# Optimization experiments

Measured on AMD Instinct MI355X. Metric: run time of the kernel, lower is better.

Reference implementation:

```python
import jax, jax.numpy as jnp
import numpy as np


def _conv(x, w, b, pad_h=0):
    # x: [B,C,H,W_feat], w: [O,C,kh,1]; kernel width is 1 so this is a 1D conv along H
    y = jax.lax.conv_general_dilated(
        x, w, window_strides=(1, 1), padding=[(pad_h, pad_h), (0, 0)],
        dimension_numbers=('NCHW', 'OIHW', 'NCHW'))
    return y + b[None, :, None, None]


def _lin(x, w, b):
    # Semi_Linear: shared nn.Linear applied to the last axis of every [channel, height] slice.
    # Since the nested loops cover the full leading dims, this is one batched matmul.
    return jnp.einsum('bchi,oi->bcho', x, w) + b


def setup_inputs() -> dict:
    key = jax.random.key(0)
    ks = jax.random.split(key, 40)
    B = 4096
    rn = lambda k, shape, s=0.1: jax.random.normal(k, shape, jnp.float32) * s
    d = {}
    d['x'] = jax.random.normal(ks[0], (B, 1, 5, 127), jnp.float32)
    # block A params (first set of definitions in __init__)
    d['ca1_w'] = rn(ks[1], (5, 1, 3, 1));    d['ca1_b'] = rn(ks[2], (5,))
    d['l01_w'] = rn(ks[3], (81, 127));        d['l01_b'] = rn(ks[4], (81,))
    d['cb1_w'] = rn(ks[5], (25, 5, 3, 1));    d['cb1_b'] = rn(ks[6], (25,))
    d['cc1_w'] = rn(ks[7], (25, 1, 1, 1));    d['cc1_b'] = rn(ks[8], (25,))
    d['r01_w'] = rn(ks[9], (81, 127));        d['r01_b'] = rn(ks[10], (81,))
    # block B params
    d['c1_w'] = rn(ks[11], (75, 25, 2, 1));   d['c1_b'] = rn(ks[12], (75,))
    d['l1_w'] = rn(ks[13], (30, 81));         d['l1_b'] = rn(ks[14], (30,))
    d['c2_w'] = rn(ks[15], (125, 75, 2, 1));  d['c2_b'] = rn(ks[16], (125,))
    d['ca_w'] = rn(ks[17], (125, 25, 3, 1));  d['ca_b'] = rn(ks[18], (125,))
    d['ra_w'] = rn(ks[19], (30, 81));         d['ra_b'] = rn(ks[20], (30,))
    # block C params (second, overriding set of definitions)
    d['ca2_w'] = rn(ks[21], (25, 125, 2, 1)); d['ca2_b'] = rn(ks[22], (25,))
    d['l02_w'] = rn(ks[23], (10, 30));        d['l02_b'] = rn(ks[24], (10,))
    d['cb2_w'] = rn(ks[25], (1, 25, 2, 1));   d['cb2_b'] = rn(ks[26], (1,))
    d['cc2_w'] = rn(ks[27], (1, 125, 1, 1));  d['cc2_b'] = rn(ks[28], (1,))
    d['r02_w'] = rn(ks[29], (10, 30));        d['r02_b'] = rn(ks[30], (10,))
    d['fl_w'] = rn(ks[31], (1, 10));          d['fl_b'] = rn(ks[32], (1,))
    return d


def reference(x, ca1_w, ca1_b, l01_w, l01_b, cb1_w, cb1_b, cc1_w, cc1_b, r01_w, r01_b,
              c1_w, c1_b, l1_w, l1_b, c2_w, c2_b, ca_w, ca_b, ra_w, ra_b,
              ca2_w, ca2_b, l02_w, l02_b, cb2_w, cb2_b, cc2_w, cc2_b, r02_w, r02_b,
              fl_w, fl_b):
    # block A
    z = _conv(x, ca1_w, ca1_b, pad_h=1)            # [B,5,5,127]
    z = jax.nn.relu(_lin(z, l01_w, l01_b))         # [B,5,5,81]
    z = _conv(z, cb1_w, cb1_b, pad_h=1)            # [B,25,5,81]
    y = _lin(x, r01_w, r01_b)                      # [B,1,5,81]
    y = _conv(y, cc1_w, cc1_b)                     # [B,25,5,81]
    x1 = z + y
    # block B
    z = _conv(x1, c1_w, c1_b)                      # [B,75,4,81]
    z = jax.nn.relu(_lin(z, l1_w, l1_b))           # [B,75,4,30]
    z = _conv(z, c2_w, c2_b)                       # [B,125,3,30]
    y = _lin(x1, ra_w, ra_b)                       # [B,25,5,30]
    y = _conv(y, ca_w, ca_b)                       # [B,125,3,30]
    x2 = z + y
    # block C
    z = _conv(x2, ca2_w, ca2_b)                    # [B,25,2,30]
    z = jax.nn.relu(_lin(z, l02_w, l02_b))         # [B,25,2,10]
    z = _conv(z, cb2_w, cb2_b)                     # [B,1,1,10]
    y = _lin(x2, r02_w, r02_b)                     # [B,125,3,10]
    y = _conv(y, cc2_w, cc2_b)                     # [B,1,3,10]
    x3 = z + y                                     # broadcast -> [B,1,3,10]
    return _lin(x3, fl_w, fl_b)                    # [B,1,3,1]
```

## Files before the change

kernel.cpp:

```cpp
#include <hip/hip_runtime.h>


typedef unsigned short u16;
typedef __attribute__((ext_vector_type(8))) short bf16x8;
typedef __attribute__((ext_vector_type(4))) float f32x4;
typedef __attribute__((ext_vector_type(8))) unsigned short u16x8;
typedef __attribute__((ext_vector_type(2))) unsigned int u32x2;

__device__ __forceinline__ float bf2f(u16 u) {
  return __uint_as_float(((unsigned)u) << 16);
}
__device__ __forceinline__ u16 f2bf(float f) {
  unsigned u = __float_as_uint(f);
  return (u16)((u + 0x7FFFu + ((u >> 16) & 1u)) >> 16);
}

#define Z4 make_float4(0.f, 0.f, 0.f, 0.f)

#define OF_CS01   0
#define OF_CS1    81
#define OF_CSR    111
#define OF_CSAC   141
#define OF_CS02   266
#define OF_CSCC2  276
#define OF_L01T   280
#define OF_R01T   10948
#define OF_SWT    21616
#define OF_CB1T   26800
#define OF_C1T    27175
#define OF_SCT    30928
#define OF_CA2T   31528
#define OF_WT2    41528
#define OF_ZPAD   57912
#define F32_TOTAL 57920

#define R_XT   0
#define R_XL   635
#define R_YA   1040
#define R_ZA   1445
#define R_P    3470
#define R_Q    4970
#define R_V4A  5270
#define R_V1   11270
#define R_VRP  12770
#define R_TP   16520
#define R_X2   0
#define R_XJ   12770
#define ROWS_TOTAL 25520

struct Ctx {
  const float *x, *ca1_w, *ca1_b, *l01_b, *r01_b, *cb1_b, *cc1_w, *cc1_b;
  const float *c1_b, *l1_b, *c2_b, *ca_b, *ra_b, *ca2_b, *l02_b;
  const float *cb2_w, *cb2_b, *cc2_w, *cc2_b, *r02_b, *fl_w, *fl_b;
  const float *l01_w, *r01_w, *l1_w, *ra_w, *c1_w, *c2_w, *ca_w, *cb1_w;
  const float *l02_w, *r02_w, *ca2_w;
  float *F;
  float *zAcc;
  float *yAcc;
  u16 *A;
  float *out;
  int CB;
  int b0g;
};

__global__ __launch_bounds__(256) void k0c(Ctx C) {
  const int t0 = blockIdx.x * 256 + threadIdx.x;
  const int NT = 32 * 256;
  float* F = C.F;
  for (int k = t0; k < 277; k += NT) {
    float s = 0.f;
    if (k < 81)       { for (int i = 0; i < 127; ++i) s += C.l01_w[k * 127 + i]; F[OF_CS01 + k] = s; }
    else if (k < 111) { int j = k - 81;  for (int a = 0; a < 81; ++a) s += C.l1_w[j * 81 + a]; F[OF_CS1 + j] = s; }
    else if (k < 141) { int j = k - 111; for (int a = 0; a < 81; ++a) s += C.ra_w[j * 81 + a]; F[OF_CSR + j] = s; }
    else if (k < 266) { int o = k - 141; for (int i = 0; i < 75; ++i) s += C.ca_w[o * 75 + i]; F[OF_CSAC + o] = s; }
    else if (k < 276) { int q = k - 266; for (int j = 0; j < 30; ++j) s += C.l02_w[q * 30 + j]; F[OF_CS02 + q] = s; }
    else              { float ss = 0.f; for (int o = 0; o < 125; ++o) ss += C.cc2_w[o]; F[OF_CSCC2] = ss; }
  }
  for (int e = t0; e < 8; e += NT) F[OF_ZPAD + e] = 0.f;
  for (int e = t0; e < 10668; e += NT) { int i = e / 84, a = e % 84;
    F[OF_L01T + e] = (a < 81) ? C.l01_w[a * 127 + i] : 0.f; }
  for (int e = t0; e < 10668; e += NT) { int i = e / 84, a = e % 84;
    F[OF_R01T + e] = (a < 81) ? C.r01_w[a * 127 + i] : 0.f; }
  for (int e = t0; e < 5184; e += NT)  { int a = e / 64, j2 = e % 64;
    F[OF_SWT + e] = (j2 < 30) ? C.l1_w[j2 * 81 + a]
                  : (j2 < 60) ? C.ra_w[(j2 - 30) * 81 + a] : 0.f; }
  for (int e = t0; e < 375; e += NT)   { int k = e / 25, c = e % 25; F[OF_CB1T + e] = C.cb1_w[c * 15 + k]; }
  for (int e = t0; e < 3750; e += NT)  { int k = e / 75, m = e % 75; F[OF_C1T + e] = C.c1_w[m * 50 + k]; }
  for (int e = t0; e < 600; e += NT)   { int j = e / 20, q2 = e % 20;
    F[OF_SCT + e] = (q2 < 10) ? C.l02_w[q2 * 30 + j] : C.r02_w[(q2 - 10) * 30 + j]; }
  for (int e = t0; e < 10000; e += NT) { int k = e / 40, r = e % 40, cg = r / 8, i = r % 8;
    F[OF_CA2T + e] = (i < 5) ? C.ca2_w[(cg * 5 + i) * 250 + k] : 0.f; }
  u16* WT2 = (u16*)(F + OF_WT2);
  for (int e = t0; e < 32768; e += NT) {
    int o = e >> 8, k = e & 255;
    float v = 0.f;
    if (o < 125) {
      if (k < 150) v = C.c2_w[o * 150 + k];
      else if (k >= 160 && k < 235) v = C.ca_w[o * 75 + (k - 160)];
    }
    WT2[e] = f2bf(v);
  }
}

__global__ __launch_bounds__(256) void k0t(Ctx C) {
  __shared__ float tile[64][65];
  const int tid = threadIdx.x;
  const int b0 = blockIdx.x * 64;
  const int i0 = blockIdx.y * 64;
  for (int e = tid; e < 64 * 64; e += 256) {
    int s = e >> 6, ii = e & 63, gi = i0 + ii;
    if (gi < 635) tile[s][ii] = C.x[(size_t)(C.b0g + b0 + s) * 635 + gi];
  }
  __syncthreads();
  const int lane = tid & 63, wv = tid >> 6;
  u16* xT = C.A + (size_t)R_XT * C.CB;
#pragma unroll
  for (int k = 0; k < 16; ++k) {
    int r = wv * 16 + k, gi = i0 + r;
    if (gi < 635) xT[(size_t)gi * C.CB + b0 + lane] = f2bf(tile[lane][r]);
  }
}

__global__ __launch_bounds__(256) void k1(Ctx C) {
  const int col = blockIdx.x * 256 + threadIdx.x;
  if (col >= C.CB) return;
  const int g = blockIdx.y, type = g / 15, r = g % 15, h = r / 3, a0 = (r % 3) * 28;
  const size_t cb = (size_t)C.CB;
  const u16* __restrict__ xT = C.A + (size_t)R_XT * cb;
  const float* __restrict__ wT = C.F + (type ? OF_R01T : OF_L01T) + a0;
  float4 A0=Z4,A1=Z4,A2=Z4,A3=Z4,A4=Z4,A5=Z4,A6=Z4;
  for (int i = 0; i < 127; ++i) {
    float xv = bf2f(xT[(size_t)(h * 127 + i) * cb + col]);
    const float4* __restrict__ W = (const float4*)(wT + i * 84);
#define K1F(Aq, P) { float4 w = W[P]; Aq.x += w.x*xv; Aq.y += w.y*xv; Aq.z += w.z*xv; Aq.w += w.w*xv; }
    K1F(A0,0) K1F(A1,1) K1F(A2,2) K1F(A3,3) K1F(A4,4) K1F(A5,5) K1F(A6,6)
#undef K1F
  }
  u16* dst = C.A + (size_t)(type ? R_YA : R_XL) * cb;
  auto wr = [&](int a, float v) {
    if (a < 81) {
      float rr = v + (type ? C.r01_b[a] : 0.f);
      dst[(size_t)(h * 81 + a) * cb + col] = f2bf(rr);
    }
  };
#define K1O(Aq, P) { wr(a0+4*P+0, Aq.x); wr(a0+4*P+1, Aq.y); wr(a0+4*P+2, Aq.z); wr(a0+4*P+3, Aq.w); }
  K1O(A0,0) K1O(A1,1) K1O(A2,2) K1O(A3,3) K1O(A4,4) K1O(A5,5) K1O(A6,6)
#undef K1O
}

__global__ __launch_bounds__(256) void k2(Ctx C) {
  const int col = blockIdx.x * 256 + threadIdx.x;
  if (col >= C.CB) return;
  const int g = blockIdx.y, c5 = g / 15, r = g % 15, h = r / 3, a0 = (r % 3) * 27;
  const u16* __restrict__ XL = C.A + (size_t)R_XL * C.CB;
  const float* __restrict__ F = C.F;
  float acc[27];
  float cb = C.ca1_b[c5];
#pragma unroll
  for (int a = 0; a < 27; ++a) acc[a] = cb * F[OF_CS01 + a0 + a] + C.l01_b[a0 + a];
#pragma unroll
  for (int dh = 0; dh < 3; ++dh) {
    int hp = h - 1 + dh;
    if (hp < 0 || hp > 4) continue;
    float w = C.ca1_w[c5 * 3 + dh];
#pragma unroll
    for (int a = 0; a < 27; ++a) acc[a] += w * bf2f(XL[(size_t)(hp * 81 + a0 + a) * C.CB + col]);
  }
  u16* zA = C.A + (size_t)R_ZA * C.CB;
#pragma unroll
  for (int a = 0; a < 27; ++a)
    zA[(size_t)((c5 * 5 + h) * 81 + a0 + a) * C.CB + col] = f2bf(fmaxf(acc[a], 0.f));
}

__global__ __launch_bounds__(256) void k3(Ctx C) {
  const int col = blockIdx.x * 256 + threadIdx.x;
  if (col >= C.CB) return;
  const int g = blockIdx.y, pair = g >> 1, j0 = (g & 1) * 32;
  const bool isP = (pair < 25);
  const size_t cb = (size_t)C.CB;
  const u16* __restrict__ src = C.A + (size_t)(isP ? (R_ZA + pair * 81) : (R_YA + (pair - 25) * 81)) * cb;
  const float* __restrict__ SWT = C.F + OF_SWT + j0;
  float4 A0=Z4,A1=Z4,A2=Z4,A3=Z4,A4=Z4,A5=Z4,A6=Z4,A7=Z4;
  for (int a = 0; a < 81; ++a) {
    float xv = bf2f(src[(size_t)a * cb + col]);
    const float4* __restrict__ W = (const float4*)(SWT + a * 64);
#define K3F(Aq, P) { float4 w = W[P]; Aq.x += w.x*xv; Aq.y += w.y*xv; Aq.z += w.z*xv; Aq.w += w.w*xv; }
    K3F(A0,0) K3F(A1,1) K3F(A2,2) K3F(A3,3) K3F(A4,4) K3F(A5,5) K3F(A6,6) K3F(A7,7)
#undef K3F
  }
  u16* dst = C.A + (size_t)(isP ? (R_P + pair * 60) : (R_Q + (pair - 25) * 60)) * cb;
  auto wr = [&](int j2, float v) {
    if (j2 < 60) dst[(size_t)j2 * cb + col] = f2bf(v);
  };
#define K3O(Aq, P) { wr(j0+4*P+0, Aq.x); wr(j0+4*P+1, Aq.y); wr(j0+4*P+2, Aq.z); wr(j0+4*P+3, Aq.w); }
  K3O(A0,0) K3O(A1,1) K3O(A2,2) K3O(A3,3) K3O(A4,4) K3O(A5,5) K3O(A6,6) K3O(A7,7)
#undef K3O
}

__global__ __launch_bounds__(256) void k4(Ctx C) {
  const int col = blockIdx.x * 256 + threadIdx.x;
  if (col >= C.CB) return;
  const int g = blockIdx.y, cg = g / 60, j2 = g % 60;
  const size_t cb = (size_t)C.CB;
  const u16* __restrict__ Pb = C.A + (size_t)R_P * cb;
  const u16* __restrict__ Qb = C.A + (size_t)R_Q * cb;
  const float* __restrict__ F = C.F;
  float sj = (j2 < 30) ? F[OF_CS1 + j2] : F[OF_CSR + (j2 - 30)];
  float acc[5][5];
#pragma unroll
  for (int cl = 0; cl < 5; ++cl) {
    int c = cg * 5 + cl;
    float base = (C.cb1_b[c] + C.cc1_b[c]) * sj;
    float cw = C.cc1_w[c];
#pragma unroll
    for (int h = 0; h < 5; ++h)
      acc[cl][h] = base + cw * bf2f(Qb[(size_t)(h * 60 + j2) * cb + col]);
  }
#pragma unroll
  for (int c5 = 0; c5 < 5; ++c5)
#pragma unroll
    for (int hp = 0; hp < 5; ++hp) {
      float pv = bf2f(Pb[(size_t)((c5 * 5 + hp) * 60 + j2) * cb + col]);
#pragma unroll
      for (int dh = 0; dh < 3; ++dh) {
        int h = hp + 1 - dh;
        if (h < 0 || h > 4) continue;
        const float* __restrict__ w = F + OF_CB1T + (c5 * 3 + dh) * 25 + cg * 5;
#pragma unroll
        for (int cl = 0; cl < 5; ++cl) acc[cl][h] += w[cl] * pv;
      }
    }
  u16* v4 = C.A + (size_t)R_V4A * cb;
  u16* v1 = C.A + (size_t)R_V1 * cb;
#pragma unroll
  for (int cl = 0; cl < 5; ++cl) {
    int row = (cg * 5 + cl) * 60 + j2;
    ushort4 pk;
    pk.x = f2bf(acc[cl][0]); pk.y = f2bf(acc[cl][1]);
    pk.z = f2bf(acc[cl][2]); pk.w = f2bf(acc[cl][3]);
    *(ushort4*)(v4 + ((size_t)row * cb + col) * 4) = pk;
    v1[(size_t)row * cb + col] = f2bf(acc[cl][4]);
  }
  if (j2 >= 30) {
    u16* vrp = C.A + (size_t)R_VRP * cb;
    int jr = j2 - 30;
#pragma unroll
    for (int cl = 0; cl < 5; ++cl) {
      int base = (cg * 5 + cl) * 30 + jr;
      vrp[(size_t)(base)        * cb + col] = f2bf(acc[cl][0]);
      vrp[(size_t)(base + 750)  * cb + col] = f2bf(acc[cl][1]);
      vrp[(size_t)(base + 1500) * cb + col] = f2bf(acc[cl][2]);
      vrp[(size_t)(base + 2250) * cb + col] = f2bf(acc[cl][3]);
      vrp[(size_t)(base + 3000) * cb + col] = f2bf(acc[cl][4]);
    }
  }
}

__global__ __launch_bounds__(256, 2) void k5(Ctx C) {
  const int col = blockIdx.x * 256 + threadIdx.x;
  if (col >= C.CB) return;
  const int g = blockIdx.y, mg = g / 30, j = g % 30;
  const size_t cb = (size_t)C.CB;
  const u16* __restrict__ v4 = C.A + (size_t)R_V4A * cb;
  const u16* __restrict__ v1 = C.A + (size_t)R_V1 * cb;
  const float* __restrict__ F = C.F;
  float s1 = F[OF_CS1 + j], lb = C.l1_b[j];
  float4 B0,B1,B2,B3,B4,B5,B6,B7,B8,B9,B10,B11,B12,B13,B14;
#define K5I(Bq, P) { float bb = C.c1_b[mg*15+P] * s1 + lb; Bq = make_float4(bb,bb,bb,bb); }
  K5I(B0,0) K5I(B1,1) K5I(B2,2) K5I(B3,3) K5I(B4,4) K5I(B5,5) K5I(B6,6) K5I(B7,7)
  K5I(B8,8) K5I(B9,9) K5I(B10,10) K5I(B11,11) K5I(B12,12) K5I(B13,13) K5I(B14,14)
#undef K5I
  for (int c = 0; c < 25; ++c) {
    int row = c * 60 + j;
    ushort4 pk = *(const ushort4*)(v4 + ((size_t)row * cb + col) * 4);
    float x0 = bf2f(pk.x), x1 = bf2f(pk.y), x2 = bf2f(pk.z), x3 = bf2f(pk.w);
    float x4 = bf2f(v1[(size_t)row * cb + col]);
    const float* __restrict__ wp0 = F + OF_C1T + (c * 2) * 75 + mg * 15;
    const float* __restrict__ wp1 = wp0 + 75;
#define K5F(Bq, P) { float w0v = wp0[P], w1v = wp1[P]; \
    Bq.x += w0v*x0 + w1v*x1; Bq.y += w0v*x1 + w1v*x2; \
    Bq.z += w0v*x2 + w1v*x3; Bq.w += w0v*x3 + w1v*x4; }
    K5F(B0,0) K5F(B1,1) K5F(B2,2) K5F(B3,3) K5F(B4,4) K5F(B5,5) K5F(B6,6) K5F(B7,7)
    K5F(B8,8) K5F(B9,9) K5F(B10,10) K5F(B11,11) K5F(B12,12) K5F(B13,13) K5F(B14,14)
#undef K5F
  }
  u16* tp = C.A + (size_t)R_TP * cb;
#define K5O(Bq, P) { int rb = (mg*15+P)*30 + j; \
    tp[(size_t)(rb)        * cb + col] = f2bf(fmaxf(Bq.x, 0.f)); \
    tp[(size_t)(rb + 2250) * cb + col] = f2bf(fmaxf(Bq.y, 0.f)); \
    tp[(size_t)(rb + 4500) * cb + col] = f2bf(fmaxf(Bq.z, 0.f)); \
    tp[(size_t)(rb + 6750) * cb + col] = f2bf(fmaxf(Bq.w, 0.f)); }
  K5O(B0,0) K5O(B1,1) K5O(B2,2) K5O(B3,3) K5O(B4,4) K5O(B5,5) K5O(B6,6) K5O(B7,7)
  K5O(B8,8) K5O(B9,9) K5O(B10,10) K5O(B11,11) K5O(B12,12) K5O(B13,13) K5O(B14,14)
#undef K5O
}

union CvtAF { u32x2 p[2]; bf16x8 v; };

#define RD(D, TA, OFF) asm volatile("ds_read_b64_tr_b16 %0, %1 offset:" OFF : "=&v"(D) : "v"(TA));
#define TRS_EVEN(TA) \
  RD(p00,TA,"0")     RD(p01,TA,"1024")  RD(p10,TA,"8192")  RD(p11,TA,"9216") \
  RD(p20,TA,"16384") RD(p21,TA,"17408") RD(p30,TA,"24576") RD(p31,TA,"25600") \
  RD(p40,TA,"32768") RD(p41,TA,"33792") RD(p50,TA,"40960") RD(p51,TA,"41984") \
  RD(p60,TA,"49152") RD(p61,TA,"50176") RD(p70,TA,"57344") RD(p71,TA,"58368")
#define TRS_ODD(TA) \
  RD(p00,TA,"128")   RD(p01,TA,"1152")  RD(p10,TA,"8320")  RD(p11,TA,"9344") \
  RD(p20,TA,"16512") RD(p21,TA,"17536") RD(p30,TA,"24704") RD(p31,TA,"25728") \
  RD(p40,TA,"32896") RD(p41,TA,"33920") RD(p50,TA,"41088") RD(p51,TA,"42112") \
  RD(p60,TA,"49280") RD(p61,TA,"50304") RD(p70,TA,"57472") RD(p71,TA,"58496")

__global__ __launch_bounds__(256, 2) void k6m(Ctx C) {
  __shared__ u16 sA[32768];
  const int tid = threadIdx.x;
  const int col0 = blockIdx.x * 128;
  const int gy = blockIdx.y;
  const int j = gy / 3, h3 = gy % 3;
  const size_t cb = (size_t)C.CB;
  const u16* __restrict__ A_ = C.A;
  const u16* __restrict__ WT2 = (const u16*)(C.F + OF_WT2);
  const float* __restrict__ F = C.F;

  const int x = tid & 63, wv = tid >> 6;
  const int klane = (x >> 1) & 3;
  const int m0s = ((x >> 3) << 4) + ((x & 1) << 3);
  const u16* zsrc = (const u16*)(F + OF_ZPAD);
#pragma unroll
  for (int p = 0; p < 16; ++p) {
    int k = p * 16 + wv * 4 + klane;
    const u16* src;
    bool pad = (k >= 150 && k < 160) || (k >= 235);
    if (pad) {
      src = zsrc;
    } else {
      int srow;
      if (k < 150) srow = R_TP + (h3 + (k & 1)) * 2250 + (k >> 1) * 30 + j;
      else { int kk = k - 160; int c = kk / 3; srow = R_VRP + (h3 + (kk - c * 3)) * 750 + c * 30 + j; }
      src = A_ + (size_t)srow * cb + col0 + m0s;
    }
    __builtin_amdgcn_global_load_lds(
        (const __attribute__((address_space(1))) void*)src,
        (__attribute__((address_space(3))) void*)&sA[(p * 4 + wv) * 512],
        16, 0, 0);
  }

  const int l = tid & 63, w = tid >> 6;
  const int lc = l & 15, q = l >> 4;
  const u16* wbA = WT2 + (size_t)(w * 32 + lc) * 256 + q * 8;
  const u16* wbB = WT2 + (size_t)(w * 32 + 16 + lc) * 256 + q * 8;
  bf16x8 b00 = *(const bf16x8*)(wbA + 0*32), b01 = *(const bf16x8*)(wbA + 1*32),
         b02 = *(const bf16x8*)(wbA + 2*32), b03 = *(const bf16x8*)(wbA + 3*32),
         b04 = *(const bf16x8*)(wbA + 4*32), b05 = *(const bf16x8*)(wbA + 5*32),
         b06 = *(const bf16x8*)(wbA + 6*32), b07 = *(const bf16x8*)(wbA + 7*32);
  bf16x8 b10 = *(const bf16x8*)(wbB + 0*32), b11 = *(const bf16x8*)(wbB + 1*32),
         b12 = *(const bf16x8*)(wbB + 2*32), b13 = *(const bf16x8*)(wbB + 3*32),
         b14 = *(const bf16x8*)(wbB + 4*32), b15 = *(const bf16x8*)(wbB + 5*32),
         b16 = *(const bf16x8*)(wbB + 6*32), b17 = *(const bf16x8*)(wbB + 7*32);

  float rbj = C.ra_b[j];
  u16* x2b = C.A + (size_t)R_X2 * cb;
  const size_t rowbase = (size_t)(h3 * 30 + j) * 125;
  const int o0 = w * 32 + lc;
  const int o1 = o0 + 16;
  const int o1c = (o1 < 125) ? o1 : 0;
  float bs0 = C.c2_b[o0] + C.ca_b[o0] + rbj * F[OF_CSAC + o0];
  float bs1 = C.c2_b[o1c] + C.ca_b[o1c] + rbj * F[OF_CSAC + o1c];

  __syncthreads();

  unsigned ldsbase = (unsigned)(size_t)(&sA[0]);
  const unsigned ta0 = ldsbase + (unsigned)((2 * q) * 1024 + lc * 8);
  const unsigned ta1 = ta0 + 256;
  const unsigned ta2 = ta0 + 512;
  const unsigned ta3 = ta0 + 768;

  u32x2 p00,p01, p10,p11, p20,p21, p30,p31, p40,p41, p50,p51, p60,p61, p70,p71;

  TRS_EVEN(ta0)

#define MM(FS, BA, BB) \
    a0 = __builtin_amdgcn_mfma_f32_16x16x32_bf16(FS, BA, a0, 0, 0, 0); \
    a1 = __builtin_amdgcn_mfma_f32_16x16x32_bf16(FS, BB, a1, 0, 0, 0);

#define MG_BODY(MG, ...) { \
    asm volatile("s_waitcnt lgkmcnt(0)" ::: "memory"); \
    __builtin_amdgcn_sched_barrier(0); \
    bf16x8 f0,f1,f2,f3,f4,f5,f6,f7; \
    { CvtAF c_; c_.p[0]=p00; c_.p[1]=p01; f0=c_.v; } \
    { CvtAF c_; c_.p[0]=p10; c_.p[1]=p11; f1=c_.v; } \
    { CvtAF c_; c_.p[0]=p20; c_.p[1]=p21; f2=c_.v; } \
    { CvtAF c_; c_.p[0]=p30; c_.p[1]=p31; f3=c_.v; } \
    { CvtAF c_; c_.p[0]=p40; c_.p[1]=p41; f4=c_.v; } \
    { CvtAF c_; c_.p[0]=p50; c_.p[1]=p51; f5=c_.v; } \
    { CvtAF c_; c_.p[0]=p60; c_.p[1]=p61; f6=c_.v; } \
    { CvtAF c_; c_.p[0]=p70; c_.p[1]=p71; f7=c_.v; } \
    __VA_ARGS__ \
    f32x4 a0 = {0.f,0.f,0.f,0.f}, a1 = {0.f,0.f,0.f,0.f}; \
    MM(f0,b00,b10) MM(f1,b01,b11) MM(f2,b02,b12) MM(f3,b03,b13) \
    MM(f4,b04,b14) MM(f5,b05,b15) MM(f6,b06,b16) MM(f7,b07,b17) \
    const int cw = col0 + (MG) * 16 + q * 4; \
    { ushort4 pk; pk.x = f2bf(a0[0]+bs0); pk.y = f2bf(a0[1]+bs0); \
      pk.z = f2bf(a0[2]+bs0); pk.w = f2bf(a0[3]+bs0); \
      *(ushort4*)(x2b + (rowbase + o0) * cb + cw) = pk; } \
    if (o1 < 125) { ushort4 pk; pk.x = f2bf(a1[0]+bs1); pk.y = f2bf(a1[1]+bs1); \
      pk.z = f2bf(a1[2]+bs1); pk.w = f2bf(a1[3]+bs1); \
      *(ushort4*)(x2b + (rowbase + o1) * cb + cw) = pk; } \
  }

  MG_BODY(0, TRS_ODD(ta0))
  MG_BODY(1, TRS_EVEN(ta1))
  MG_BODY(2, TRS_ODD(ta1))
  MG_BODY(3, TRS_EVEN(ta2))
  MG_BODY(4, TRS_ODD(ta2))
  MG_BODY(5, TRS_EVEN(ta3))
  MG_BODY(6, TRS_ODD(ta3))
  MG_BODY(7)
#undef MG_BODY
#undef MM
}

__global__ __launch_bounds__(256) void k7(Ctx C) {
  const int col = blockIdx.x * 256 + threadIdx.x;
  if (col >= C.CB) return;
  const int g = blockIdx.y;
  const int o = g / 3, h3 = g % 3;
  const size_t cb = (size_t)C.CB;
  const u16* __restrict__ x2b = C.A + (size_t)R_X2 * cb;
  const float* __restrict__ SCT = C.F + OF_SCT;
  float4 A0=Z4,A1=Z4,A2=Z4,A3=Z4,A4=Z4;
  for (int j = 0; j < 30; ++j) {
    float xv = bf2f(x2b[(size_t)((h3 * 30 + j) * 125 + o) * cb + col]);
    const float4* __restrict__ W = (const float4*)(SCT + j * 20);
#define K7F(Aq, P) { float4 w = W[P]; Aq.x += w.x*xv; Aq.y += w.y*xv; Aq.z += w.z*xv; Aq.w += w.w*xv; }
    K7F(A0,0) K7F(A1,1) K7F(A2,2) K7F(A3,3) K7F(A4,4)
#undef K7F
  }
  u16* XJ = C.A + (size_t)R_XJ * cb;
  auto wq = [&](int qq, float v) { XJ[(size_t)(g * 10 + qq) * cb + col] = f2bf(v); };
  wq(0,A0.x); wq(1,A0.y); wq(2,A0.z); wq(3,A0.w);
  wq(4,A1.x); wq(5,A1.y); wq(6,A1.z); wq(7,A1.w);
  wq(8,A2.x); wq(9,A2.y);
  float s = C.fl_w[0]*A2.z + C.fl_w[1]*A2.w
          + C.fl_w[2]*A3.x + C.fl_w[3]*A3.y + C.fl_w[4]*A3.z + C.fl_w[5]*A3.w
          + C.fl_w[6]*A4.x + C.fl_w[7]*A4.y + C.fl_w[8]*A4.z + C.fl_w[9]*A4.w;
  atomicAdd(&C.yAcc[(size_t)h3 * C.CB + col], C.cc2_w[o] * s);
}

__global__ __launch_bounds__(256) void k8a(Ctx C) {
  const int col = blockIdx.x * 256 + threadIdx.x;
  if (col >= C.CB) return;
  const int g = blockIdx.y, cg = g / 20, rem = g % 20, hh = rem / 10, q = rem % 10;
  const size_t cb = (size_t)C.CB;
  const u16* __restrict__ XJ = C.A + (size_t)R_XJ * cb;
  const float* __restrict__ F = C.F;
  float4 A0 = Z4; float a4 = 0.f;
  const float* __restrict__ Wb = F + OF_CA2T + cg * 8;
  for (int k = 0; k < 250; ++k) {
    int o = k >> 1, dh = k & 1;
    float xv = bf2f(XJ[(size_t)((o * 3 + hh + dh) * 10 + q) * cb + col]);
    const float* __restrict__ wr = Wb + k * 40;
    float4 w0 = *(const float4*)wr;
    float w4 = wr[4];
    A0.x += w0.x * xv; A0.y += w0.y * xv; A0.z += w0.z * xv; A0.w += w0.w * xv;
    a4 += w4 * xv;
  }
  float s02 = F[OF_CS02 + q];
  float lb = C.l02_b[q];
  const int c0 = cg * 5;
  float part = 0.f;
  {
    float zc;
    zc = fmaxf(A0.x + C.ca2_b[c0+0] * s02 + lb, 0.f); part += C.cb2_w[(c0+0)*2+hh] * zc;
    zc = fmaxf(A0.y + C.ca2_b[c0+1] * s02 + lb, 0.f); part += C.cb2_w[(c0+1)*2+hh] * zc;
    zc = fmaxf(A0.z + C.ca2_b[c0+2] * s02 + lb, 0.f); part += C.cb2_w[(c0+2)*2+hh] * zc;
    zc = fmaxf(A0.w + C.ca2_b[c0+3] * s02 + lb, 0.f); part += C.cb2_w[(c0+3)*2+hh] * zc;
    zc = fmaxf(a4   + C.ca2_b[c0+4] * s02 + lb, 0.f); part += C.cb2_w[(c0+4)*2+hh] * zc;
  }
  atomicAdd(&C.zAcc[col], C.fl_w[q] * part);
}

__global__ __launch_bounds__(256) void k8c(Ctx C) {
  const int col = blockIdx.x * 256 + threadIdx.x;
  if (col >= C.CB) return;
  float scc2 = C.F[OF_CSCC2];
  float cst = C.fl_b[0];
#pragma unroll
  for (int q = 0; q < 10; ++q)
    cst += C.fl_w[q] * (C.cb2_b[0] + C.r02_b[q] * scc2 + C.cc2_b[0]);
  float za = C.zAcc[col];
#pragma unroll
  for (int h = 0; h < 3; ++h)
    C.out[(size_t)(C.b0g + col) * 3 + h] = cst + za + C.yAcc[(size_t)h * C.CB + col];
}

extern "C" void kernel_launch(void* const* d_in, const int* in_sizes, int n_in,
                              void* d_out, int out_size, void* d_ws, size_t ws_size,
                              hipStream_t stream) {
  (void)n_in; (void)out_size;
  Ctx C;
  C.x     = (const float*)d_in[0];
  C.ca1_w = (const float*)d_in[1];  C.ca1_b = (const float*)d_in[2];
  C.l01_w = (const float*)d_in[3];  C.l01_b = (const float*)d_in[4];
  C.cb1_w = (const float*)d_in[5];  C.cb1_b = (const float*)d_in[6];
  C.cc1_w = (const float*)d_in[7];  C.cc1_b = (const float*)d_in[8];
  C.r01_w = (const float*)d_in[9];  C.r01_b = (const float*)d_in[10];
  C.c1_w  = (const float*)d_in[11]; C.c1_b  = (const float*)d_in[12];
  C.l1_w  = (const float*)d_in[13]; C.l1_b  = (const float*)d_in[14];
  C.c2_w  = (const float*)d_in[15]; C.c2_b  = (const float*)d_in[16];
  C.ca_w  = (const float*)d_in[17]; C.ca_b  = (const float*)d_in[18];
  C.ra_w  = (const float*)d_in[19]; C.ra_b  = (const float*)d_in[20];
  C.ca2_w = (const float*)d_in[21]; C.ca2_b = (const float*)d_in[22];
  C.l02_w = (const float*)d_in[23]; C.l02_b = (const float*)d_in[24];
  C.cb2_w = (const float*)d_in[25]; C.cb2_b = (const float*)d_in[26];
  C.cc2_w = (const float*)d_in[27]; C.cc2_b = (const float*)d_in[28];
  C.r02_w = (const float*)d_in[29]; C.r02_b = (const float*)d_in[30];
  C.fl_w  = (const float*)d_in[31]; C.fl_b  = (const float*)d_in[32];
  C.out   = (float*)d_out;

  const int B = in_sizes[0] / 635;

  int CB = 4096;
  if (CB > B) CB = B;
  size_t accoff, actoff;
  for (;;) {
    accoff = ((size_t)F32_TOTAL * 4 + 255) & ~(size_t)255;
    actoff = (accoff + (size_t)4 * CB * 4 + 255) & ~(size_t)255;
    if (CB <= 256 || actoff + (size_t)ROWS_TOTAL * CB * 2 <= ws_size) break;
    CB >>= 1;
  }
  C.F = (float*)d_ws;
  C.zAcc = (float*)((char*)d_ws + accoff);
  C.yAcc = C.zAcc + CB;
  C.A = (u16*)((char*)d_ws + actoff);
  C.CB = CB;

  C.b0g = 0;
  k0c<<<dim3(32), dim3(256), 0, stream>>>(C);

  const int bt64 = CB / 64, bt128 = CB / 128, bt256 = (CB + 255) / 256;
  for (int b0 = 0; b0 < B; b0 += CB) {
    C.b0g = b0;
    hipMemsetAsync(C.zAcc, 0, (size_t)4 * CB * sizeof(float), stream);
    k0t<<<dim3(bt64, 10),   dim3(256), 0, stream>>>(C);
    k1 <<<dim3(bt256, 30),  dim3(256), 0, stream>>>(C);
    k2 <<<dim3(bt256, 75),  dim3(256), 0, stream>>>(C);
    k3 <<<dim3(bt256, 60),  dim3(256), 0, stream>>>(C);
    k4 <<<dim3(bt256, 300), dim3(256), 0, stream>>>(C);
    k5 <<<dim3(bt256, 150), dim3(256), 0, stream>>>(C);
    k6m<<<dim3(bt128, 90),  dim3(256), 0, stream>>>(C);
    k7 <<<dim3(bt256, 375), dim3(256), 0, stream>>>(C);
    k8a<<<dim3(bt256, 100), dim3(256), 0, stream>>>(C);
    k8c<<<dim3(bt256, 1),   dim3(256), 0, stream>>>(C);
  }
}
```

Baseline: 324.8 us.

## Port block-B first conv (k5) to bf16 MFMA with LDS transposed reads

Replaces the scalar FMA implementation of the c1 conv (25->75 channels, kernel 2) with an MFMA-based kernel. Each block handles one (j, output-height) pair and 128 batch columns, and stages its 64-row K slab into LDS with global_load_lds. The slab is read back through ds_read_b64_tr_b16 and multiplied against prepacked bf16 c1 weights. The upstream k4 output layout changes to a single h-major VLP buffer, so the K rows for each output height are contiguous. This adds weight prepacking and K padding from 50 to 64, and wastes some MFMA work on padded output channels 75..79.

```diff
diff --git a/kernel.cpp b/kernel.cpp
--- a/kernel.cpp
+++ b/kernel.cpp
@@ -32,7 +32,8 @@
 #define OF_CA2T   31528
 #define OF_WT2    41528
 #define OF_ZPAD   57912
-#define F32_TOTAL 57920
+#define OF_C1W2   57920
+#define F32_TOTAL 60480
 
 #define R_XT   0
 #define R_XL   635
@@ -40,8 +41,7 @@
 #define R_ZA   1445
 #define R_P    3470
 #define R_Q    4970
-#define R_V4A  5270
-#define R_V1   11270
+#define R_VLP  5270
 #define R_VRP  12770
 #define R_TP   16520
 #define R_X2   0
@@ -85,7 +85,6 @@
     F[OF_SWT + e] = (j2 < 30) ? C.l1_w[j2 * 81 + a]
                   : (j2 < 60) ? C.ra_w[(j2 - 30) * 81 + a] : 0.f; }
   for (int e = t0; e < 375; e += NT)   { int k = e / 25, c = e % 25; F[OF_CB1T + e] = C.cb1_w[c * 15 + k]; }
-  for (int e = t0; e < 3750; e += NT)  { int k = e / 75, m = e % 75; F[OF_C1T + e] = C.c1_w[m * 50 + k]; }
   for (int e = t0; e < 600; e += NT)   { int j = e / 20, q2 = e % 20;
     F[OF_SCT + e] = (q2 < 10) ? C.l02_w[q2 * 30 + j] : C.r02_w[(q2 - 10) * 30 + j]; }
   for (int e = t0; e < 10000; e += NT) { int k = e / 40, r = e % 40, cg = r / 8, i = r % 8;
@@ -99,6 +98,12 @@
       else if (k >= 160 && k < 235) v = C.ca_w[o * 75 + (k - 160)];
     }
     WT2[e] = f2bf(v);
+  }
+  u16* C1W2 = (u16*)(F + OF_C1W2);
+  for (int e = t0; e < 5120; e += NT) {
+    int o = e >> 6, k = e & 63;
+    float v = (o < 75 && k < 50) ? C.c1_w[o * 50 + k] : 0.f;
+    C1W2[e] = f2bf(v);
   }
 }
 
@@ -230,72 +235,124 @@
         for (int cl = 0; cl < 5; ++cl) acc[cl][h] += w[cl] * pv;
       }
     }
-  u16* v4 = C.A + (size_t)R_V4A * cb;
-  u16* v1 = C.A + (size_t)R_V1 * cb;
-#pragma unroll
-  for (int cl = 0; cl < 5; ++cl) {
-    int row = (cg * 5 + cl) * 60 + j2;
-    ushort4 pk;
-    pk.x = f2bf(acc[cl][0]); pk.y = f2bf(acc[cl][1]);
-    pk.z = f2bf(acc[cl][2]); pk.w = f2bf(acc[cl][3]);
-    *(ushort4*)(v4 + ((size_t)row * cb + col) * 4) = pk;
-    v1[(size_t)row * cb + col] = f2bf(acc[cl][4]);
-  }
-  if (j2 >= 30) {
+  if (j2 < 30) {
+    u16* vlp = C.A + (size_t)R_VLP * cb;
+#pragma unroll
+    for (int cl = 0; cl < 5; ++cl) {
+      int base = (cg * 5 + cl) * 30 + j2;
+#pragma unroll
+      for (int h = 0; h < 5; ++h)
+        vlp[(size_t)(base + h * 750) * cb + col] = f2bf(acc[cl][h]);
+    }
+  } else {
     u16* vrp = C.A + (size_t)R_VRP * cb;
     int jr = j2 - 30;
 #pragma unroll
     for (int cl = 0; cl < 5; ++cl) {
       int base = (cg * 5 + cl) * 30 + jr;
-      vrp[(size_t)(base)        * cb + col] = f2bf(acc[cl][0]);
-      vrp[(size_t)(base + 750)  * cb + col] = f2bf(acc[cl][1]);
-      vrp[(size_t)(base + 1500) * cb + col] = f2bf(acc[cl][2]);
-      vrp[(size_t)(base + 2250) * cb + col] = f2bf(acc[cl][3]);
-      vrp[(size_t)(base + 3000) * cb + col] = f2bf(acc[cl][4]);
+#pragma unroll
+      for (int h = 0; h < 5; ++h)
+        vrp[(size_t)(base + h * 750) * cb + col] = f2bf(acc[cl][h]);
     }
   }
 }
 
-__global__ __launch_bounds__(256, 2) void k5(Ctx C) {
-  const int col = blockIdx.x * 256 + threadIdx.x;
-  if (col >= C.CB) return;
-  const int g = blockIdx.y, mg = g / 30, j = g % 30;
+union CvtAF { u32x2 p[2]; bf16x8 v; };
+
+__global__ __launch_bounds__(256, 2) void k5m(Ctx C) {
+  __shared__ u16 sA[8192];
+  const int tid = threadIdx.x;
+  const int col0 = blockIdx.x * 128;
+  const int gy = blockIdx.y;
+  const int j = gy >> 2, h4 = gy & 3;
   const size_t cb = (size_t)C.CB;
-  const u16* __restrict__ v4 = C.A + (size_t)R_V4A * cb;
-  const u16* __restrict__ v1 = C.A + (size_t)R_V1 * cb;
+  const u16* __restrict__ A_ = C.A;
+  const u16* __restrict__ WB = (const u16*)(C.F + OF_C1W2);
   const float* __restrict__ F = C.F;
+
+  const int x = tid & 63, wv = tid >> 6;
+  const int klane = (x >> 1) & 3;
+  const int m0s = ((x >> 3) << 4) + ((x & 1) << 3);
+  const u16* zsrc = (const u16*)(F + OF_ZPAD);
+#pragma unroll
+  for (int p = 0; p < 4; ++p) {
+    int k = p * 16 + wv * 4 + klane;
+    const u16* src;
+    if (k >= 50) {
+      src = zsrc;
+    } else {
+      int c = k >> 1, dc = k & 1;
+      int srow = R_VLP + (h4 + dc) * 750 + c * 30 + j;
+      src = A_ + (size_t)srow * cb + col0 + m0s;
+    }
+    __builtin_amdgcn_global_load_lds(
+        (const __attribute__((address_space(1))) void*)src,
+        (__attribute__((address_space(3))) void*)&sA[(p * 4 + wv) * 512],
+        16, 0, 0);
+  }
+
+  const int l = tid & 63, w = tid >> 6;
+  const int lc = l & 15, q = l >> 4;
+#define BF(N, S) (*(const bf16x8*)(WB + (size_t)((N)*16 + lc) * 64 + (S)*32 + q*8))
+  bf16x8 B00 = BF(0,0), B10 = BF(1,0), B20 = BF(2,0), B30 = BF(3,0), B40 = BF(4,0);
+  bf16x8 B01 = BF(0,1), B11 = BF(1,1), B21 = BF(2,1), B31 = BF(3,1), B41 = BF(4,1);
+#undef BF
   float s1 = F[OF_CS1 + j], lb = C.l1_b[j];
-  float4 B0,B1,B2,B3,B4,B5,B6,B7,B8,B9,B10,B11,B12,B13,B14;
-#define K5I(Bq, P) { float bb = C.c1_b[mg*15+P] * s1 + lb; Bq = make_float4(bb,bb,bb,bb); }
-  K5I(B0,0) K5I(B1,1) K5I(B2,2) K5I(B3,3) K5I(B4,4) K5I(B5,5) K5I(B6,6) K5I(B7,7)
-  K5I(B8,8) K5I(B9,9) K5I(B10,10) K5I(B11,11) K5I(B12,12) K5I(B13,13) K5I(B14,14)
-#undef K5I
-  for (int c = 0; c < 25; ++c) {
-    int row = c * 60 + j;
-    ushort4 pk = *(const ushort4*)(v4 + ((size_t)row * cb + col) * 4);
-    float x0 = bf2f(pk.x), x1 = bf2f(pk.y), x2 = bf2f(pk.z), x3 = bf2f(pk.w);
-    float x4 = bf2f(v1[(size_t)row * cb + col]);
-    const float* __restrict__ wp0 = F + OF_C1T + (c * 2) * 75 + mg * 15;
-    const float* __restrict__ wp1 = wp0 + 75;
-#define K5F(Bq, P) { float w0v = wp0[P], w1v = wp1[P]; \
-    Bq.x += w0v*x0 + w1v*x1; Bq.y += w0v*x1 + w1v*x2; \
-    Bq.z += w0v*x2 + w1v*x3; Bq.w += w0v*x3 + w1v*x4; }
-    K5F(B0,0) K5F(B1,1) K5F(B2,2) K5F(B3,3) K5F(B4,4) K5F(B5,5) K5F(B6,6) K5F(B7,7)
-    K5F(B8,8) K5F(B9,9) K5F(B10,10) K5F(B11,11) K5F(B12,12) K5F(B13,13) K5F(B14,14)
-#undef K5F
-  }
+  const int o4r = 64 + lc;
+  const int o4c = (o4r < 75) ? o4r : 0;
+  float bs0 = C.c1_b[lc] * s1 + lb;
+  float bs1 = C.c1_b[16 + lc] * s1 + lb;
+  float bs2 = C.c1_b[32 + lc] * s1 + lb;
+  float bs3 = C.c1_b[48 + lc] * s1 + lb;
+  float bs4 = C.c1_b[o4c] * s1 + lb;
+
+  __syncthreads();
+
+  unsigned ldsbase = (unsigned)(size_t)(&sA[0]);
+  unsigned ta = ldsbase + (unsigned)((2 * q) * 1024 + w * 256 + lc * 8);
+
+  u32x2 e00,e01,e02,e03, e10,e11,e12,e13;
+  asm volatile("ds_read_b64_tr_b16 %0, %1"             : "=&v"(e00) : "v"(ta));
+  asm volatile("ds_read_b64_tr_b16 %0, %1 offset:1024" : "=&v"(e01) : "v"(ta));
+  asm volatile("ds_read_b64_tr_b16 %0, %1 offset:8192" : "=&v"(e02) : "v"(ta));
+  asm volatile("ds_read_b64_tr_b16 %0, %1 offset:9216" : "=&v"(e03) : "v"(ta));
+  asm volatile("ds_read_b64_tr_b16 %0, %1 offset:128"  : "=&v"(e10) : "v"(ta));
+  asm volatile("ds_read_b64_tr_b16 %0, %1 offset:1152" : "=&v"(e11) : "v"(ta));
+  asm volatile("ds_read_b64_tr_b16 %0, %1 offset:8320" : "=&v"(e12) : "v"(ta));
+  asm volatile("ds_read_b64_tr_b16 %0, %1 offset:9344" : "=&v"(e13) : "v"(ta));
+  asm volatile("s_waitcnt lgkmcnt(0)" ::: "memory");
+  __builtin_amdgcn_sched_barrier(0);
+
+  bf16x8 f0s0, f0s1, f1s0, f1s1;
+  { CvtAF c_; c_.p[0]=e00; c_.p[1]=e01; f0s0=c_.v; }
+  { CvtAF c_; c_.p[0]=e02; c_.p[1]=e03; f0s1=c_.v; }
+  { CvtAF c_; c_.p[0]=e10; c_.p[1]=e11; f1s0=c_.v; }
+  { CvtAF c_; c_.p[0]=e12; c_.p[1]=e13; f1s1=c_.v; }
+
+  f32x4 a00={0,0,0,0},a01={0,0,0,0},a02={0,0,0,0},a03={0,0,0,0},a04={0,0,0,0};
+  f32x4 a10={0,0,0,0},a11={0,0,0,0},a12={0,0,0,0},a13={0,0,0,0},a14={0,0,0,0};
+#define MF(AC, FA, BB) AC = __builtin_amdgcn_mfma_f32_16x16x32_bf16(FA, BB, AC, 0, 0, 0);
+  MF(a00,f0s0,B00) MF(a01,f0s0,B10) MF(a02,f0s0,B20) MF(a03,f0s0,B30) MF(a04,f0s0,B40)
+  MF(a10,f1s0,B00) MF(a11,f1s0,B10) MF(a12,f1s0,B20) MF(a13,f1s0,B30) MF(a14,f1s0,B40)
+  MF(a00,f0s1,B01) MF(a01,f0s1,B11) MF(a02,f0s1,B21) MF(a03,f0s1,B31) MF(a04,f0s1,B41)
+  MF(a10,f1s1,B01) MF(a11,f1s1,B11) MF(a12,f1s1,B21) MF(a13,f1s1,B31) MF(a14,f1s1,B41)
+#undef MF
+
   u16* tp = C.A + (size_t)R_TP * cb;
-#define K5O(Bq, P) { int rb = (mg*15+P)*30 + j; \
-    tp[(size_t)(rb)        * cb + col] = f2bf(fmaxf(Bq.x, 0.f)); \
-    tp[(size_t)(rb + 2250) * cb + col] = f2bf(fmaxf(Bq.y, 0.f)); \
-    tp[(size_t)(rb + 4500) * cb + col] = f2bf(fmaxf(Bq.z, 0.f)); \
-    tp[(size_t)(rb + 6750) * cb + col] = f2bf(fmaxf(Bq.w, 0.f)); }
-  K5O(B0,0) K5O(B1,1) K5O(B2,2) K5O(B3,3) K5O(B4,4) K5O(B5,5) K5O(B6,6) K5O(B7,7)
-  K5O(B8,8) K5O(B9,9) K5O(B10,10) K5O(B11,11) K5O(B12,12) K5O(B13,13) K5O(B14,14)
-#undef K5O
-}
-
-union CvtAF { u32x2 p[2]; bf16x8 v; };
+  const int cw0 = col0 + 2 * w * 16 + q * 4;
+#define ST(AC, O, BS, CW) { int o_ = (O); if (o_ < 75) { \
+    size_t rw = (size_t)(h4 * 2250 + o_ * 30 + j) * cb + (CW); \
+    ushort4 pk; pk.x = f2bf(fmaxf(AC[0]+(BS),0.f)); pk.y = f2bf(fmaxf(AC[1]+(BS),0.f)); \
+    pk.z = f2bf(fmaxf(AC[2]+(BS),0.f)); pk.w = f2bf(fmaxf(AC[3]+(BS),0.f)); \
+    *(ushort4*)(tp + rw) = pk; } }
+  ST(a00, lc,      bs0, cw0)      ST(a01, 16 + lc, bs1, cw0)
+  ST(a02, 32 + lc, bs2, cw0)      ST(a03, 48 + lc, bs3, cw0)
+  ST(a04, 64 + lc, bs4, cw0)
+  ST(a10, lc,      bs0, cw0 + 16) ST(a11, 16 + lc, bs1, cw0 + 16)
+  ST(a12, 32 + lc, bs2, cw0 + 16) ST(a13, 48 + lc, bs3, cw0 + 16)
+  ST(a14, 64 + lc, bs4, cw0 + 16)
+#undef ST
+}
 
 #define RD(D, TA, OFF) asm volatile("ds_read_b64_tr_b16 %0, %1 offset:" OFF : "=&v"(D) : "v"(TA));
 #define TRS_EVEN(TA) \
@@ -545,7 +602,7 @@
     k2 <<<dim3(bt256, 75),  dim3(256), 0, stream>>>(C);
     k3 <<<dim3(bt256, 60),  dim3(256), 0, stream>>>(C);
     k4 <<<dim3(bt256, 300), dim3(256), 0, stream>>>(C);
-    k5 <<<dim3(bt256, 150), dim3(256), 0, stream>>>(C);
+    k5m<<<dim3(bt128, 120), dim3(256), 0, stream>>>(C);
     k6m<<<dim3(bt128, 90),  dim3(256), 0, stream>>>(C);
     k7 <<<dim3(bt256, 375), dim3(256), 0, stream>>>(C);
     k8a<<<dim3(bt256, 100), dim3(256), 0, stream>>>(C);
```

Result: faster. 304.3 us, median of 3 (-6.3%).
